# Kernel optimization log

Hardware: AMD Instinct MI355X
Metric: run time of the kernel (lower is better)

## Reference

```python
import jax, jax.numpy as jnp
import numpy as np
from jax import lax

SEQ, B, NF, NC, D, NO, L = 2036, 32, 64, 100, 512, 4, 2048
EPS = 1e-5


def leaky(x):
    return jnp.where(x > 0, x, 0.2 * x)


def conv1d(x, w, b):
    # x: [B, Cin, L], w: [Cout, Cin, K] -> [B, Cout, L-K+1] (VALID)
    y = lax.conv_general_dilated(x, w, (1,), 'VALID',
                                 dimension_numbers=('NCH', 'OIH', 'NCH'))
    return y + b[None, :, None]


def maxpool3(x):
    # kernel 3, stride 1, VALID, over last dim
    return lax.reduce_window(x, -jnp.inf, lax.max, (1, 1, 3), (1, 1, 1), 'VALID')


def layernorm(x, g, b):
    m = jnp.mean(x, -1, keepdims=True)
    v = jnp.mean(jnp.square(x - m), -1, keepdims=True)
    return (x - m) * lax.rsqrt(v + EPS) * g + b


def setup_inputs() -> dict:
    key = jax.random.key(0)
    ks = jax.random.split(key, 16)
    s = 0.02
    return {
        'input': jax.random.normal(ks[0], (SEQ, B, NF), jnp.float32),
        'history': jax.random.normal(ks[1], (B, NO, L), jnp.float32),
        'static': jax.random.normal(ks[2], (B, NC), jnp.float32),
        'W_feat': jax.random.normal(ks[3], (D, NF), jnp.float32) * s,
        'b_feat': jnp.zeros((D,), jnp.float32),
        'w1': jax.random.normal(ks[4], (D // 4, NO, 3), jnp.float32) * s,
        'b1': jnp.zeros((D // 4,), jnp.float32),
        'w2': jax.random.normal(ks[5], (D // 2, D // 4, 3), jnp.float32) * s,
        'b2': jnp.zeros((D // 2,), jnp.float32),
        'w3': jax.random.normal(ks[6], (D, D // 2, 3), jnp.float32) * s,
        'b3': jnp.zeros((D,), jnp.float32),
        'g1': jnp.ones((D,), jnp.float32),
        'beta1': jnp.zeros((D,), jnp.float32),
        'W_city': jax.random.normal(ks[7], (D, NC), jnp.float32) * s,
        'b_city': jnp.zeros((D,), jnp.float32),
        'g2': jnp.ones((D,), jnp.float32),
        'beta2': jnp.zeros((D,), jnp.float32),
    }


def reference(input, history, static, W_feat, b_feat, w1, b1, w2, b2, w3, b3,
              g1, beta1, W_city, b_city, g2, beta2):
    # feat embed: [S, B, NF] @ [NF, D]
    x = leaky(jnp.einsum('sbf,df->sbd', input, W_feat) + b_feat)
    # conv/pool stack on history [B, NO, L]
    h = maxpool3(leaky(conv1d(history, w1, b1)))
    h = maxpool3(leaky(conv1d(h, w2, b2)))
    h = maxpool3(leaky(conv1d(h, w3, b3)))            # [B, D, S]
    x = x + jnp.transpose(h, (2, 0, 1))               # [S, B, D]
    x = layernorm(x, g1, beta1)
    # diag_embed(city_embed(static)) matmul == broadcasted elementwise scale
    c = static @ W_city.T + b_city                    # [B, D]
    x = x * c[None, :, :]
    x = layernorm(x, g2, beta2)
    return x
```

## Files before the change

kernel.cpp:

```cpp
#include <hip/hip_runtime.h>
#include <hip/hip_bf16.h>

#define SEQ 2036
#define BB 32
#define DDIM 512

typedef __attribute__((ext_vector_type(4))) float f32x4;
typedef __attribute__((ext_vector_type(8))) short bf16x8v;
typedef __attribute__((ext_vector_type(8))) unsigned short u16x8;
typedef __attribute__((ext_vector_type(4))) unsigned short u16x4;

__device__ __forceinline__ float leaky_f(float x) { return x > 0.f ? x : 0.2f * x; }
__device__ __forceinline__ unsigned short f2bf(float x) {
    unsigned u = __float_as_uint(x);
    return (unsigned short)((u + 0x7fffu + ((u >> 16) & 1u)) >> 16);
}
__device__ __forceinline__ float bf2f(unsigned short h) { return __uint_as_float(((unsigned)h) << 16); }

#define GLOAD_LDS16(g, l)                                                                  \
    __builtin_amdgcn_global_load_lds((__attribute__((address_space(1))) const unsigned int*)(g), \
                                     (__attribute__((address_space(3))) unsigned int*)(l), 16, 0, 0)

__global__ void transpose_w_kernel(const float* __restrict__ w, float* __restrict__ wT,
                                   int Dout, int K3) {
    int i = blockIdx.x * blockDim.x + threadIdx.x;
    if (i < Dout * K3) {
        int d = i / K3, k = i - d * K3;
        wT[k * Dout + d] = w[i];
    }
}

__global__ void prep_w_kernel(const float* __restrict__ w, __hip_bfloat16* __restrict__ wp,
                              int CIN, int NB) {
    int idx = blockIdx.x * 256 + threadIdx.x;
    int NQ = CIN >> 5;
    int total = 3 * NQ * NB * 4096;
    if (idx >= total) return;
    int o = idx & 4095, tile = idx >> 12;
    int nb = tile % NB;
    int tmp = tile / NB;
    int q = tmp % NQ, k = tmp / NQ;
    int n = o >> 5, low = o & 31;
    int cs = low >> 3, j = low & 7;
    int c = cs ^ ((n >> 1) & 3);
    int kk = (c << 3) | j;
    float v = w[((size_t)(nb * 128 + n)) * CIN * 3 + (q * 32 + kk) * 3 + k];
    ((unsigned short*)wp)[idx] = f2bf(v);
}

__global__ void prep_wf_kernel(const float* __restrict__ Wf, __hip_bfloat16* __restrict__ wfP) {
    int idx = blockIdx.x * 256 + threadIdx.x;
    int e = idx & 7;
    int l = (idx >> 3) & 63;
    int frag = idx >> 9;
    int q = frag >> 5, j = frag & 31;
    int n = l & 15, g = l >> 4;
    ((unsigned short*)wfP)[idx] = f2bf(Wf[(j * 16 + n) * 64 + q * 32 + g * 8 + e]);
}

__global__ void city_kernel(const float* __restrict__ st, const float* __restrict__ Wc,
                            const float* __restrict__ bc, float* __restrict__ c) {
    int b = blockIdx.x, d = threadIdx.x;
    const float* sb = st + b * 100;
    float acc = bc[d];
#pragma unroll 4
    for (int f = 0; f < 100; ++f) acc = fmaf(sb[f], Wc[d * 100 + f], acc);
    c[b * DDIM + d] = acc;
}

__global__ __launch_bounds__(128) void conv1_kernel(const float* __restrict__ in,
                                                    const float* __restrict__ wT,
                                                    const float* __restrict__ bias,
                                                    __hip_bfloat16* __restrict__ out) {
    const int b = blockIdx.y, s0 = blockIdx.x * 32, d = threadIdx.x;
    __shared__ float tile[4][36];
    const float* inb = in + (size_t)b * 4 * 2048;
    for (int i = threadIdx.x; i < 4 * 36; i += 128) {
        int cin = i / 36, p = i - cin * 36;
        int s = s0 + p;
        tile[cin][p] = (s < 2048) ? inb[cin * 2048 + s] : 0.f;
    }
    __syncthreads();
    float acc[34];
#pragma unroll
    for (int i = 0; i < 34; ++i) acc[i] = 0.f;
#pragma unroll
    for (int cin = 0; cin < 4; ++cin) {
        float w0 = wT[(cin * 3 + 0) * 128 + d];
        float w1 = wT[(cin * 3 + 1) * 128 + d];
        float w2 = wT[(cin * 3 + 2) * 128 + d];
        float r0 = tile[cin][0], r1 = tile[cin][1];
#pragma unroll
        for (int p = 0; p < 34; ++p) {
            float r2 = tile[cin][p + 2];
            acc[p] = fmaf(r0, w0, fmaf(r1, w1, fmaf(r2, w2, acc[p])));
            r0 = r1; r1 = r2;
        }
    }
    float bvv = bias[d];
    unsigned short* o16 = (unsigned short*)out;
#pragma unroll
    for (int i = 0; i < 32; ++i) {
        int sp = s0 + i;
        if (sp < 2044) {
            float v = leaky_f(fmaxf(fmaxf(acc[i], acc[i + 1]), acc[i + 2]) + bvv);
            o16[((size_t)b * 2044 + sp) * 128 + d] = f2bf(v);
        }
    }
}

template <int CIN, int DOUT>
__global__ __launch_bounds__(256, 3) void conv_mfma_kernel(
    const __hip_bfloat16* __restrict__ hin,
    const __hip_bfloat16* __restrict__ wprep,
    const float* __restrict__ bias,
    __hip_bfloat16* __restrict__ hout,
    int Lin, int Lpool, long bstride, long sstride)
{
    constexpr int NQ = CIN / 32;
    constexpr int HALVES = (CIN + 127) / 128;
    constexpr int NSTEP = 3 * NQ;
    constexpr int SPH = NSTEP / HALVES;
    constexpr int NBL = DOUT / 128;

    __shared__ __attribute__((aligned(16))) unsigned char smem[34816 + 16384];
    unsigned char* panel = smem;
    unsigned char* cstage = smem;
    unsigned char* bls = smem + 34816;

    const int t = threadIdx.x;
    const int lane = t & 63, w = t >> 6;
    const int wr = w >> 1, wn = w & 1;
    const int l15 = lane & 15, lg = lane >> 4;

    const int nwg = gridDim.x;
    const int lw = (blockIdx.x & 7) * (nwg >> 3) + (blockIdx.x >> 3);
    const int nb = lw % NBL;
    const int tmp = lw / NBL;
    const int st = tmp % 17;
    const int b = tmp / 17;
    const int s0 = st * 126;

    auto stage_panel = [&](int half) {
        const char* srcb = (const char*)hin + (((size_t)b * Lin) * CIN + half * 128) * 2;
#pragma unroll
        for (int iter = 0; iter < 8; ++iter) {
            int chunk = iter * 256 + t;
            int r = chunk >> 4, cd = chunk & 15;
            int c = (cd & 8) | ((cd ^ r) & 7);
            int row = s0 + r; if (row > Lin - 1) row = Lin - 1;
            const char* src = srcb + ((size_t)row * CIN + c * 8) * 2;
            GLOAD_LDS16(src, panel + (iter * 256 + w * 64) * 16);
        }
        if (t < 32) {
            int chunk = 2048 + t;
            int r = chunk >> 4, cd = chunk & 15;
            int c = (cd & 8) | ((cd ^ r) & 7);
            int row = s0 + r; if (row > Lin - 1) row = Lin - 1;
            const char* src = srcb + ((size_t)row * CIN + c * 8) * 2;
            GLOAD_LDS16(src, panel + 2048 * 16);
        }
    };
    auto stage_b = [&](int ss, int bi) {
        int k = (ss % SPH) >> 2;
        int qg = (ss / SPH) * 4 + (ss & 3);
        int tile = (k * NQ + qg) * NBL + nb;
        const char* src = (const char*)wprep + (size_t)tile * 8192;
        char* dst = (char*)bls + bi * 8192;
        GLOAD_LDS16(src + t * 16, dst + (w << 10));
        GLOAD_LDS16(src + 4096 + t * 16, dst + 4096 + (w << 10));
    };

    f32x4 acc[4][4];
#pragma unroll
    for (int i = 0; i < 4; ++i)
#pragma unroll
        for (int j = 0; j < 4; ++j) acc[i][j] = (f32x4){0.f, 0.f, 0.f, 0.f};

    stage_panel(0);
    stage_b(0, 0);
    __syncthreads();

    int boff[4];
#pragma unroll
    for (int nf = 0; nf < 4; ++nf) {
        int n = wn * 64 + nf * 16 + l15;
        boff[nf] = n * 64 + ((lg ^ ((n >> 1) & 3)) << 4);
    }
    const int rbse = wr * 64 + l15;

    for (int ss = 0; ss < NSTEP; ++ss) {
        const int bi = ss & 1;
        if (ss + 1 < NSTEP) stage_b(ss + 1, bi ^ 1);
        const int k = (ss % SPH) >> 2;
        const int cc = (ss & 3) * 4 + lg;
        bf16x8v a[4], bfr[4];
#pragma unroll
        for (int mf = 0; mf < 4; ++mf) {
            int r = rbse + mf * 16 + k;
            int csw = (cc & 8) | ((cc ^ r) & 7);
            a[mf] = *(const bf16x8v*)(panel + r * 256 + (csw << 4));
        }
#pragma unroll
        for (int nf = 0; nf < 4; ++nf)
            bfr[nf] = *(const bf16x8v*)(bls + bi * 8192 + boff[nf]);
#pragma unroll
        for (int mf = 0; mf < 4; ++mf)
#pragma unroll
            for (int nf = 0; nf < 4; ++nf)
                acc[mf][nf] = __builtin_amdgcn_mfma_f32_16x16x32_bf16(a[mf], bfr[nf], acc[mf][nf], 0, 0, 0);
        __syncthreads();
        if (HALVES == 2 && ss == SPH - 1) {
            stage_panel(1);
            __syncthreads();
        }
    }

#pragma unroll
    for (int mf = 0; mf < 4; ++mf) {
        int srow = wr * 64 + mf * 16 + (lg << 2);
#pragma unroll
        for (int nf = 0; nf < 4; ++nf) {
            int n = wn * 64 + nf * 16 + l15;
            f32x4 v = acc[mf][nf];
            unsigned lo = (unsigned)f2bf(v.x) | ((unsigned)f2bf(v.y) << 16);
            unsigned hi = (unsigned)f2bf(v.z) | ((unsigned)f2bf(v.w) << 16);
            *(uint2*)(cstage + (size_t)n * 272 + srow * 2) = make_uint2(lo, hi);
        }
    }
    __syncthreads();

    const int n = t & 127, h = t >> 7;
    const float bv = bias[nb * 128 + n];
    const int SP = (Lpool - s0 < 126) ? (Lpool - s0) : 126;
    const int splo = h ? 63 : 0;
    const int sphim = h ? 126 : 63;
    const int sphi = (SP < sphim) ? SP : sphim;
    const int cbg = h ? 7 : 0, ceg = h ? 16 : 9;
    unsigned short* outp = (unsigned short*)hout;
    const size_t obase = (size_t)b * bstride + (size_t)s0 * sstride + nb * 128 + n;
    float p2 = 0.f, p1 = 0.f;
    for (int j = cbg; j < ceg; ++j) {
        u16x8 ch = *(const u16x8*)(cstage + (size_t)n * 272 + (j << 4));
#pragma unroll
        for (int i = 0; i < 8; ++i) {
            float cur = bf2f(ch[i]);
            int sp = j * 8 + i - 2;
            if (sp >= splo && sp < sphi) {
                float v = fmaxf(fmaxf(p2, p1), cur) + bv;
                outp[obase + (size_t)sp * sstride] = f2bf(leaky_f(v));
            }
            p2 = p1; p1 = cur;
        }
    }
}

#define XSTR 514
__global__ __launch_bounds__(256, 4) void epi_mfma3_kernel(
    const float* __restrict__ input,
    const __hip_bfloat16* __restrict__ wfP,
    const float* __restrict__ bfeat,
    const __hip_bfloat16* __restrict__ h3,
    const float* __restrict__ cvec,
    const float* __restrict__ g1, const float* __restrict__ be1,
    const float* __restrict__ g2, const float* __restrict__ be2,
    float* __restrict__ outp)
{
    __shared__ float x_lds[16 * XSTR];
    const int t = threadIdx.x;
    const int lane = t & 63, w = t >> 6;
    const int l15 = lane & 15, lg = lane >> 4;
    const long r0 = (long)blockIdx.x * 16;

    f32x4 acc[8];
#pragma unroll
    for (int jl = 0; jl < 8; ++jl) acc[jl] = (f32x4){0.f, 0.f, 0.f, 0.f};

    const unsigned short* wp = (const unsigned short*)wfP;
#pragma unroll
    for (int q = 0; q < 2; ++q) {
        const f32x4* ap = (const f32x4*)(input + (r0 + l15) * 64 + q * 32 + lg * 8);
        f32x4 a0 = ap[0];
        f32x4 a1 = ap[1];
        bf16x8v af;
        af[0] = (short)f2bf(a0.x); af[1] = (short)f2bf(a0.y);
        af[2] = (short)f2bf(a0.z); af[3] = (short)f2bf(a0.w);
        af[4] = (short)f2bf(a1.x); af[5] = (short)f2bf(a1.y);
        af[6] = (short)f2bf(a1.z); af[7] = (short)f2bf(a1.w);
#pragma unroll
        for (int jl = 0; jl < 8; ++jl) {
            int frag = q * 32 + w * 8 + jl;
            bf16x8v bfr = *(const bf16x8v*)(wp + ((size_t)frag * 64 + lane) * 8);
            acc[jl] = __builtin_amdgcn_mfma_f32_16x16x32_bf16(af, bfr, acc[jl], 0, 0, 0);
        }
    }

#pragma unroll
    for (int jl = 0; jl < 8; ++jl) {
        int d = (w * 8 + jl) * 16 + l15;
        float bfv = bfeat[d];
#pragma unroll
        for (int i = 0; i < 4; ++i) {
            int row = lg * 4 + i;
            x_lds[row * XSTR + d] = leaky_f(acc[jl][i] + bfv);
        }
    }
    __syncthreads();

    const unsigned short* h3u = (const unsigned short*)h3;
    const int l4 = lane * 4;
    f32x4 g1a = *(const f32x4*)(g1 + l4);
    f32x4 g1b = *(const f32x4*)(g1 + 256 + l4);
    f32x4 b1a = *(const f32x4*)(be1 + l4);
    f32x4 b1b = *(const f32x4*)(be1 + 256 + l4);
    f32x4 g2a = *(const f32x4*)(g2 + l4);
    f32x4 g2b = *(const f32x4*)(g2 + 256 + l4);
    f32x4 b2a = *(const f32x4*)(be2 + l4);
    f32x4 b2b = *(const f32x4*)(be2 + 256 + l4);

    for (int rr = 0; rr < 4; ++rr) {
        int row = w * 4 + rr;
        long r = r0 + row;
        int b = (int)(r & 31);
        f32x4 xa = *(const f32x4*)(x_lds + row * XSTR + l4);
        f32x4 xb = *(const f32x4*)(x_lds + row * XSTR + 256 + l4);
        u16x4 ha = *(const u16x4*)(h3u + r * 512 + l4);
        u16x4 hb = *(const u16x4*)(h3u + r * 512 + 256 + l4);
        float v[8];
        float s = 0.f;
#pragma unroll
        for (int e = 0; e < 4; ++e) {
            v[e] = xa[e] + bf2f(ha[e]);
            v[4 + e] = xb[e] + bf2f(hb[e]);
            s += v[e] + v[4 + e];
        }
#pragma unroll
        for (int off = 32; off; off >>= 1) s += __shfl_xor(s, off);
        float m = s * (1.f / 512.f);
        float vs = 0.f;
#pragma unroll
        for (int j = 0; j < 8; ++j) { float dd = v[j] - m; vs += dd * dd; }
#pragma unroll
        for (int off = 32; off; off >>= 1) vs += __shfl_xor(vs, off);
        float rstd = rsqrtf(vs * (1.f / 512.f) + 1e-5f);

        f32x4 ca = *(const f32x4*)(cvec + b * 512 + l4);
        f32x4 cb = *(const f32x4*)(cvec + b * 512 + 256 + l4);
        float z[8]; float s2 = 0.f;
#pragma unroll
        for (int e = 0; e < 4; ++e) {
            z[e] = ((v[e] - m) * rstd * g1a[e] + b1a[e]) * ca[e];
            z[4 + e] = ((v[4 + e] - m) * rstd * g1b[e] + b1b[e]) * cb[e];
            s2 += z[e] + z[4 + e];
        }
#pragma unroll
        for (int off = 32; off; off >>= 1) s2 += __shfl_xor(s2, off);
        float m2 = s2 * (1.f / 512.f);
        float vs2 = 0.f;
#pragma unroll
        for (int j = 0; j < 8; ++j) { float dd = z[j] - m2; vs2 += dd * dd; }
#pragma unroll
        for (int off = 32; off; off >>= 1) vs2 += __shfl_xor(vs2, off);
        float rstd2 = rsqrtf(vs2 * (1.f / 512.f) + 1e-5f);

        f32x4 oa, ob;
#pragma unroll
        for (int e = 0; e < 4; ++e) {
            oa[e] = (z[e] - m2) * rstd2 * g2a[e] + b2a[e];
            ob[e] = (z[4 + e] - m2) * rstd2 * g2b[e] + b2b[e];
        }
        __builtin_nontemporal_store(oa, (f32x4*)(outp + r * 512 + l4));
        __builtin_nontemporal_store(ob, (f32x4*)(outp + r * 512 + 256 + l4));
    }
}

extern "C" void kernel_launch(void* const* d_in, const int* in_sizes, int n_in,
                              void* d_out, int out_size, void* d_ws, size_t ws_size,
                              hipStream_t stream) {
    const float* input   = (const float*)d_in[0];
    const float* history = (const float*)d_in[1];
    const float* stat    = (const float*)d_in[2];
    const float* W_feat  = (const float*)d_in[3];
    const float* b_feat  = (const float*)d_in[4];
    const float* w1      = (const float*)d_in[5];
    const float* b1      = (const float*)d_in[6];
    const float* w2      = (const float*)d_in[7];
    const float* b2      = (const float*)d_in[8];
    const float* w3      = (const float*)d_in[9];
    const float* b3      = (const float*)d_in[10];
    const float* g1      = (const float*)d_in[11];
    const float* beta1   = (const float*)d_in[12];
    const float* W_city  = (const float*)d_in[13];
    const float* b_city  = (const float*)d_in[14];
    const float* g2      = (const float*)d_in[15];
    const float* beta2   = (const float*)d_in[16];
    float* out = (float*)d_out;

    char* wsb = (char*)d_ws;
    size_t off = 0;
    auto alloc = [&](size_t bytes) {
        void* p = wsb + off;
        off = (off + bytes + 255) & ~(size_t)255;
        return p;
    };
    __hip_bfloat16* h1  = (__hip_bfloat16*)alloc((size_t)BB * 2044 * 128 * 2);
    __hip_bfloat16* h2  = (__hip_bfloat16*)alloc((size_t)BB * 2040 * 256 * 2);
    __hip_bfloat16* h3  = (__hip_bfloat16*)alloc((size_t)SEQ * BB * 512 * 2);
    float*          cv  = (float*)alloc((size_t)BB * DDIM * 4);
    float*          w1T = (float*)alloc(12 * 128 * 4);
    __hip_bfloat16* w2P = (__hip_bfloat16*)alloc((size_t)3 * 4 * 2 * 4096 * 2);
    __hip_bfloat16* w3P = (__hip_bfloat16*)alloc((size_t)3 * 8 * 4 * 4096 * 2);
    __hip_bfloat16* wfP = (__hip_bfloat16*)alloc((size_t)64 * 512 * 2);

    transpose_w_kernel<<<(12 * 128 + 255) / 256, 256, 0, stream>>>(w1, w1T, 128, 12);
    prep_w_kernel<<<(3 * 4 * 2 * 4096) / 256, 256, 0, stream>>>(w2, w2P, 128, 2);
    prep_w_kernel<<<(3 * 8 * 4 * 4096) / 256, 256, 0, stream>>>(w3, w3P, 256, 4);
    prep_wf_kernel<<<(64 * 512) / 256, 256, 0, stream>>>(W_feat, wfP);
    city_kernel<<<BB, DDIM, 0, stream>>>(stat, W_city, b_city, cv);

    conv1_kernel<<<dim3(64, BB), 128, 0, stream>>>(history, w1T, b1, h1);
    conv_mfma_kernel<128, 256><<<17 * 2 * BB, 256, 0, stream>>>(
        h1, w2P, b2, h2, 2044, 2040, 2040L * 256, 256);
    conv_mfma_kernel<256, 512><<<17 * 4 * BB, 256, 0, stream>>>(
        h2, w3P, b3, h3, 2040, 2036, 512, 32L * 512);

    epi_mfma3_kernel<<<(SEQ * BB) / 16, 256, 0, stream>>>(
        input, wfP, b_feat, h3, cv, g1, beta1, g2, beta2, out);
}
```

Measured before the change: 179.6 us.

## Load conv weight fragments directly from global in MFMA fragment order

Pre-packs the conv2/conv3 weights into per-lane MFMA B-fragment order so each wave reads its B operands with coalesced 16-byte global loads. This removes the double-buffered LDS staging of weights and the per-k-step __syncthreads. The LDS footprint drops to the activation panel, and launch bounds rise to 4 blocks per SM for higher occupancy. The cost is that weight loads are no longer prefetched a step ahead, so each MFMA step waits on global or L2 latency, and every wave reloads its fragments through cache.

```diff
diff --git a/kernel.cpp b/kernel.cpp
--- a/kernel.cpp
+++ b/kernel.cpp
@@ -30,22 +30,25 @@
     }
 }
 
-__global__ void prep_w_kernel(const float* __restrict__ w, __hip_bfloat16* __restrict__ wp,
-                              int CIN, int NB) {
+__global__ void prep_wb_kernel(const float* __restrict__ w, __hip_bfloat16* __restrict__ wb,
+                               int CIN, int NBL, int total) {
     int idx = blockIdx.x * 256 + threadIdx.x;
+    if (idx >= total) return;
     int NQ = CIN >> 5;
-    int total = 3 * NQ * NB * 4096;
-    if (idx >= total) return;
-    int o = idx & 4095, tile = idx >> 12;
-    int nb = tile % NB;
-    int tmp = tile / NB;
-    int q = tmp % NQ, k = tmp / NQ;
-    int n = o >> 5, low = o & 31;
-    int cs = low >> 3, j = low & 7;
-    int c = cs ^ ((n >> 1) & 3);
-    int kk = (c << 3) | j;
-    float v = w[((size_t)(nb * 128 + n)) * CIN * 3 + (q * 32 + kk) * 3 + k];
-    ((unsigned short*)wp)[idx] = f2bf(v);
+    int NSTEP = 3 * NQ;
+    int HALVES = (CIN + 127) / 128;
+    int SPH = NSTEP / HALVES;
+    int e = idx & 7;
+    int l = (idx >> 3) & 63;
+    int nf = (idx >> 9) & 3;
+    int wn = (idx >> 11) & 1;
+    int rest = idx >> 12;
+    int nb = rest % NBL, ss = rest / NBL;
+    int k = (ss % SPH) >> 2;
+    int qg = (ss / SPH) * 4 + (ss & 3);
+    int n = nb * 128 + wn * 64 + nf * 16 + (l & 15);
+    int cin = qg * 32 + (l >> 4) * 8 + e;
+    ((unsigned short*)wb)[idx] = f2bf(w[(size_t)n * CIN * 3 + cin * 3 + k]);
 }
 
 __global__ void prep_wf_kernel(const float* __restrict__ Wf, __hip_bfloat16* __restrict__ wfP) {
@@ -110,9 +113,9 @@
 }
 
 template <int CIN, int DOUT>
-__global__ __launch_bounds__(256, 3) void conv_mfma_kernel(
+__global__ __launch_bounds__(256, 4) void conv_mfma_kernel(
     const __hip_bfloat16* __restrict__ hin,
-    const __hip_bfloat16* __restrict__ wprep,
+    const __hip_bfloat16* __restrict__ wb,
     const float* __restrict__ bias,
     __hip_bfloat16* __restrict__ hout,
     int Lin, int Lpool, long bstride, long sstride)
@@ -123,10 +126,9 @@
     constexpr int SPH = NSTEP / HALVES;
     constexpr int NBL = DOUT / 128;
 
-    __shared__ __attribute__((aligned(16))) unsigned char smem[34816 + 16384];
+    __shared__ __attribute__((aligned(16))) unsigned char smem[34816];
     unsigned char* panel = smem;
     unsigned char* cstage = smem;
-    unsigned char* bls = smem + 34816;
 
     const int t = threadIdx.x;
     const int lane = t & 63, w = t >> 6;
@@ -161,15 +163,6 @@
             GLOAD_LDS16(src, panel + 2048 * 16);
         }
     };
-    auto stage_b = [&](int ss, int bi) {
-        int k = (ss % SPH) >> 2;
-        int qg = (ss / SPH) * 4 + (ss & 3);
-        int tile = (k * NQ + qg) * NBL + nb;
-        const char* src = (const char*)wprep + (size_t)tile * 8192;
-        char* dst = (char*)bls + bi * 8192;
-        GLOAD_LDS16(src + t * 16, dst + (w << 10));
-        GLOAD_LDS16(src + 4096 + t * 16, dst + 4096 + (w << 10));
-    };
 
     f32x4 acc[4][4];
 #pragma unroll
@@ -177,24 +170,18 @@
 #pragma unroll
         for (int j = 0; j < 4; ++j) acc[i][j] = (f32x4){0.f, 0.f, 0.f, 0.f};
 
-    stage_panel(0);
-    stage_b(0, 0);
-    __syncthreads();
-
-    int boff[4];
-#pragma unroll
-    for (int nf = 0; nf < 4; ++nf) {
-        int n = wn * 64 + nf * 16 + l15;
-        boff[nf] = n * 64 + ((lg ^ ((n >> 1) & 3)) << 4);
-    }
     const int rbse = wr * 64 + l15;
-
-    for (int ss = 0; ss < NSTEP; ++ss) {
-        const int bi = ss & 1;
-        if (ss + 1 < NSTEP) stage_b(ss + 1, bi ^ 1);
+    const unsigned short* wbp = (const unsigned short*)wb;
+
+    auto kstep = [&](int ss) {
         const int k = (ss % SPH) >> 2;
         const int cc = (ss & 3) * 4 + lg;
+        const unsigned short* wq =
+            wbp + (((size_t)ss * NBL + nb) * 2 + wn) * 2048 + (size_t)lane * 8;
         bf16x8v a[4], bfr[4];
+#pragma unroll
+        for (int nf = 0; nf < 4; ++nf)
+            bfr[nf] = *(const bf16x8v*)(wq + nf * 512);
 #pragma unroll
         for (int mf = 0; mf < 4; ++mf) {
             int r = rbse + mf * 16 + k;
@@ -202,19 +189,22 @@
             a[mf] = *(const bf16x8v*)(panel + r * 256 + (csw << 4));
         }
 #pragma unroll
-        for (int nf = 0; nf < 4; ++nf)
-            bfr[nf] = *(const bf16x8v*)(bls + bi * 8192 + boff[nf]);
-#pragma unroll
         for (int mf = 0; mf < 4; ++mf)
 #pragma unroll
             for (int nf = 0; nf < 4; ++nf)
                 acc[mf][nf] = __builtin_amdgcn_mfma_f32_16x16x32_bf16(a[mf], bfr[nf], acc[mf][nf], 0, 0, 0);
+    };
+
+    stage_panel(0);
+    __syncthreads();
+    for (int ss = 0; ss < SPH; ++ss) kstep(ss);
+    if (HALVES == 2) {
         __syncthreads();
-        if (HALVES == 2 && ss == SPH - 1) {
-            stage_panel(1);
-            __syncthreads();
-        }
-    }
+        stage_panel(1);
+        __syncthreads();
+        for (int ss = SPH; ss < NSTEP; ++ss) kstep(ss);
+    }
+    __syncthreads();
 
 #pragma unroll
     for (int mf = 0; mf < 4; ++mf) {
@@ -408,21 +398,21 @@
     __hip_bfloat16* h3  = (__hip_bfloat16*)alloc((size_t)SEQ * BB * 512 * 2);
     float*          cv  = (float*)alloc((size_t)BB * DDIM * 4);
     float*          w1T = (float*)alloc(12 * 128 * 4);
-    __hip_bfloat16* w2P = (__hip_bfloat16*)alloc((size_t)3 * 4 * 2 * 4096 * 2);
-    __hip_bfloat16* w3P = (__hip_bfloat16*)alloc((size_t)3 * 8 * 4 * 4096 * 2);
+    __hip_bfloat16* wb2 = (__hip_bfloat16*)alloc((size_t)12 * 2 * 8 * 512 * 2);
+    __hip_bfloat16* wb3 = (__hip_bfloat16*)alloc((size_t)24 * 4 * 8 * 512 * 2);
     __hip_bfloat16* wfP = (__hip_bfloat16*)alloc((size_t)64 * 512 * 2);
 
     transpose_w_kernel<<<(12 * 128 + 255) / 256, 256, 0, stream>>>(w1, w1T, 128, 12);
-    prep_w_kernel<<<(3 * 4 * 2 * 4096) / 256, 256, 0, stream>>>(w2, w2P, 128, 2);
-    prep_w_kernel<<<(3 * 8 * 4 * 4096) / 256, 256, 0, stream>>>(w3, w3P, 256, 4);
+    prep_wb_kernel<<<(12 * 2 * 8 * 512) / 256, 256, 0, stream>>>(w2, wb2, 128, 2, 12 * 2 * 8 * 512);
+    prep_wb_kernel<<<(24 * 4 * 8 * 512) / 256, 256, 0, stream>>>(w3, wb3, 256, 4, 24 * 4 * 8 * 512);
     prep_wf_kernel<<<(64 * 512) / 256, 256, 0, stream>>>(W_feat, wfP);
     city_kernel<<<BB, DDIM, 0, stream>>>(stat, W_city, b_city, cv);
 
     conv1_kernel<<<dim3(64, BB), 128, 0, stream>>>(history, w1T, b1, h1);
     conv_mfma_kernel<128, 256><<<17 * 2 * BB, 256, 0, stream>>>(
-        h1, w2P, b2, h2, 2044, 2040, 2040L * 256, 256);
+        h1, wb2, b2, h2, 2044, 2040, 2040L * 256, 256);
     conv_mfma_kernel<256, 512><<<17 * 4 * BB, 256, 0, stream>>>(
-        h2, w3P, b3, h3, 2040, 2036, 512, 32L * 512);
+        h2, wb3, b3, h3, 2040, 2036, 512, 32L * 512);
 
     epi_mfma3_kernel<<<(SEQ * BB) / 16, 256, 0, stream>>>(
         input, wfP, b_feat, h3, cv, g1, beta1, g2, beta2, out);
```

Measured after the change: 191.6 us. 1.07x slower.

## Load conv3 weight fragments directly from global and fuse prep kernels

Applied to the files above, without the earlier changes.

Merges the five small weight-prep and city-embedding kernels into one launch, which removes launch overhead. For the conv3 layer, weights are pre-packed into per-lane MFMA fragment order and read straight from global/L2 into registers, so there is no LDS double-buffering and no per-step barrier. This frees 16 KB of LDS and raises the occupancy target to 4 blocks. The cost is that global-load latency now sits directly in front of each MFMA step, and weight reads are no longer shared through LDS across the workgroup.

```diff
diff --git a/kernel.cpp b/kernel.cpp
--- a/kernel.cpp
+++ b/kernel.cpp
@@ -21,51 +21,68 @@
     __builtin_amdgcn_global_load_lds((__attribute__((address_space(1))) const unsigned int*)(g), \
                                      (__attribute__((address_space(3))) unsigned int*)(l), 16, 0, 0)
 
-__global__ void transpose_w_kernel(const float* __restrict__ w, float* __restrict__ wT,
-                                   int Dout, int K3) {
-    int i = blockIdx.x * blockDim.x + threadIdx.x;
-    if (i < Dout * K3) {
-        int d = i / K3, k = i - d * K3;
-        wT[k * Dout + d] = w[i];
-    }
-}
-
-__global__ void prep_w_kernel(const float* __restrict__ w, __hip_bfloat16* __restrict__ wp,
-                              int CIN, int NB) {
+__global__ __launch_bounds__(256) void prep_all_kernel(
+    const float* __restrict__ w1, float* __restrict__ w1T,
+    const float* __restrict__ w2, __hip_bfloat16* __restrict__ w2P,
+    const float* __restrict__ w3, __hip_bfloat16* __restrict__ wb3,
+    const float* __restrict__ Wf, __hip_bfloat16* __restrict__ wfP,
+    const float* __restrict__ st, const float* __restrict__ Wc,
+    const float* __restrict__ bc, float* __restrict__ cv)
+{
     int idx = blockIdx.x * 256 + threadIdx.x;
-    int NQ = CIN >> 5;
-    int total = 3 * NQ * NB * 4096;
-    if (idx >= total) return;
-    int o = idx & 4095, tile = idx >> 12;
-    int nb = tile % NB;
-    int tmp = tile / NB;
-    int q = tmp % NQ, k = tmp / NQ;
-    int n = o >> 5, low = o & 31;
-    int cs = low >> 3, j = low & 7;
-    int c = cs ^ ((n >> 1) & 3);
-    int kk = (c << 3) | j;
-    float v = w[((size_t)(nb * 128 + n)) * CIN * 3 + (q * 32 + kk) * 3 + k];
-    ((unsigned short*)wp)[idx] = f2bf(v);
-}
-
-__global__ void prep_wf_kernel(const float* __restrict__ Wf, __hip_bfloat16* __restrict__ wfP) {
-    int idx = blockIdx.x * 256 + threadIdx.x;
-    int e = idx & 7;
-    int l = (idx >> 3) & 63;
-    int frag = idx >> 9;
-    int q = frag >> 5, j = frag & 31;
-    int n = l & 15, g = l >> 4;
-    ((unsigned short*)wfP)[idx] = f2bf(Wf[(j * 16 + n) * 64 + q * 32 + g * 8 + e]);
-}
-
-__global__ void city_kernel(const float* __restrict__ st, const float* __restrict__ Wc,
-                            const float* __restrict__ bc, float* __restrict__ c) {
-    int b = blockIdx.x, d = threadIdx.x;
-    const float* sb = st + b * 100;
-    float acc = bc[d];
+    if (idx < 1536) {
+        int d = idx / 12, k = idx - d * 12;
+        w1T[k * 128 + d] = w1[idx];
+        return;
+    }
+    idx -= 1536;
+    if (idx < 98304) {
+        int o = idx & 4095, tile = idx >> 12;
+        int nb = tile % 2;
+        int tmp = tile / 2;
+        int q = tmp % 4, k = tmp / 4;
+        int n = o >> 5, low = o & 31;
+        int cs = low >> 3, j = low & 7;
+        int c = cs ^ ((n >> 1) & 3);
+        int kk = (c << 3) | j;
+        float v = w2[((size_t)(nb * 128 + n)) * 128 * 3 + (q * 32 + kk) * 3 + k];
+        ((unsigned short*)w2P)[idx] = f2bf(v);
+        return;
+    }
+    idx -= 98304;
+    if (idx < 393216) {
+        int e = idx & 7;
+        int l = (idx >> 3) & 63;
+        int nf = (idx >> 9) & 3;
+        int wn = (idx >> 11) & 1;
+        int rest = idx >> 12;
+        int nb = rest % 4, ss = rest / 4;
+        int k = (ss % 12) >> 2;
+        int qg = (ss / 12) * 4 + (ss & 3);
+        int n = nb * 128 + wn * 64 + nf * 16 + (l & 15);
+        int cin = qg * 32 + (l >> 4) * 8 + e;
+        ((unsigned short*)wb3)[idx] = f2bf(w3[(size_t)n * 256 * 3 + cin * 3 + k]);
+        return;
+    }
+    idx -= 393216;
+    if (idx < 32768) {
+        int e = idx & 7;
+        int l = (idx >> 3) & 63;
+        int frag = idx >> 9;
+        int q = frag >> 5, j = frag & 31;
+        int n = l & 15, g = l >> 4;
+        ((unsigned short*)wfP)[idx] = f2bf(Wf[(j * 16 + n) * 64 + q * 32 + g * 8 + e]);
+        return;
+    }
+    idx -= 32768;
+    if (idx < 16384) {
+        int b = idx >> 9, d = idx & 511;
+        const float* sb = st + b * 100;
+        float acc = bc[d];
 #pragma unroll 4
-    for (int f = 0; f < 100; ++f) acc = fmaf(sb[f], Wc[d * 100 + f], acc);
-    c[b * DDIM + d] = acc;
+        for (int f = 0; f < 100; ++f) acc = fmaf(sb[f], Wc[d * 100 + f], acc);
+        cv[b * 512 + d] = acc;
+    }
 }
 
 __global__ __launch_bounds__(128) void conv1_kernel(const float* __restrict__ in,
@@ -109,8 +126,8 @@
     }
 }
 
-template <int CIN, int DOUT>
-__global__ __launch_bounds__(256, 3) void conv_mfma_kernel(
+template <int CIN, int DOUT, bool LDSB>
+__global__ __launch_bounds__(256, LDSB ? 3 : 4) void conv_mfma_kernel(
     const __hip_bfloat16* __restrict__ hin,
     const __hip_bfloat16* __restrict__ wprep,
     const float* __restrict__ bias,
@@ -122,8 +139,9 @@
     constexpr int NSTEP = 3 * NQ;
     constexpr int SPH = NSTEP / HALVES;
     constexpr int NBL = DOUT / 128;
-
-    __shared__ __attribute__((aligned(16))) unsigned char smem[34816 + 16384];
+    constexpr int SMEM = LDSB ? (34816 + 16384) : 34816;
+
+    __shared__ __attribute__((aligned(16))) unsigned char smem[SMEM];
     unsigned char* panel = smem;
     unsigned char* cstage = smem;
     unsigned char* bls = smem + 34816;
@@ -161,15 +179,6 @@
             GLOAD_LDS16(src, panel + 2048 * 16);
         }
     };
-    auto stage_b = [&](int ss, int bi) {
-        int k = (ss % SPH) >> 2;
-        int qg = (ss / SPH) * 4 + (ss & 3);
-        int tile = (k * NQ + qg) * NBL + nb;
-        const char* src = (const char*)wprep + (size_t)tile * 8192;
-        char* dst = (char*)bls + bi * 8192;
-        GLOAD_LDS16(src + t * 16, dst + (w << 10));
-        GLOAD_LDS16(src + 4096 + t * 16, dst + 4096 + (w << 10));
-    };
 
     f32x4 acc[4][4];
 #pragma unroll
@@ -177,43 +186,87 @@
 #pragma unroll
         for (int j = 0; j < 4; ++j) acc[i][j] = (f32x4){0.f, 0.f, 0.f, 0.f};
 
-    stage_panel(0);
-    stage_b(0, 0);
-    __syncthreads();
-
-    int boff[4];
-#pragma unroll
-    for (int nf = 0; nf < 4; ++nf) {
-        int n = wn * 64 + nf * 16 + l15;
-        boff[nf] = n * 64 + ((lg ^ ((n >> 1) & 3)) << 4);
-    }
     const int rbse = wr * 64 + l15;
 
-    for (int ss = 0; ss < NSTEP; ++ss) {
-        const int bi = ss & 1;
-        if (ss + 1 < NSTEP) stage_b(ss + 1, bi ^ 1);
-        const int k = (ss % SPH) >> 2;
-        const int cc = (ss & 3) * 4 + lg;
-        bf16x8v a[4], bfr[4];
-#pragma unroll
-        for (int mf = 0; mf < 4; ++mf) {
-            int r = rbse + mf * 16 + k;
-            int csw = (cc & 8) | ((cc ^ r) & 7);
-            a[mf] = *(const bf16x8v*)(panel + r * 256 + (csw << 4));
-        }
-#pragma unroll
-        for (int nf = 0; nf < 4; ++nf)
-            bfr[nf] = *(const bf16x8v*)(bls + bi * 8192 + boff[nf]);
-#pragma unroll
-        for (int mf = 0; mf < 4; ++mf)
+    if (LDSB) {
+        auto stage_b = [&](int ss, int bi) {
+            int k = (ss % SPH) >> 2;
+            int qg = (ss / SPH) * 4 + (ss & 3);
+            int tile = (k * NQ + qg) * NBL + nb;
+            const char* src = (const char*)wprep + (size_t)tile * 8192;
+            char* dst = (char*)bls + bi * 8192;
+            GLOAD_LDS16(src + t * 16, dst + (w << 10));
+            GLOAD_LDS16(src + 4096 + t * 16, dst + 4096 + (w << 10));
+        };
+        stage_panel(0);
+        stage_b(0, 0);
+        __syncthreads();
+        int boff[4];
+#pragma unroll
+        for (int nf = 0; nf < 4; ++nf) {
+            int n = wn * 64 + nf * 16 + l15;
+            boff[nf] = n * 64 + ((lg ^ ((n >> 1) & 3)) << 4);
+        }
+        for (int ss = 0; ss < NSTEP; ++ss) {
+            const int bi = ss & 1;
+            if (ss + 1 < NSTEP) stage_b(ss + 1, bi ^ 1);
+            const int k = (ss % SPH) >> 2;
+            const int cc = (ss & 3) * 4 + lg;
+            bf16x8v a[4], bfr[4];
+#pragma unroll
+            for (int mf = 0; mf < 4; ++mf) {
+                int r = rbse + mf * 16 + k;
+                int csw = (cc & 8) | ((cc ^ r) & 7);
+                a[mf] = *(const bf16x8v*)(panel + r * 256 + (csw << 4));
+            }
 #pragma unroll
             for (int nf = 0; nf < 4; ++nf)
-                acc[mf][nf] = __builtin_amdgcn_mfma_f32_16x16x32_bf16(a[mf], bfr[nf], acc[mf][nf], 0, 0, 0);
+                bfr[nf] = *(const bf16x8v*)(bls + bi * 8192 + boff[nf]);
+#pragma unroll
+            for (int mf = 0; mf < 4; ++mf)
+#pragma unroll
+                for (int nf = 0; nf < 4; ++nf)
+                    acc[mf][nf] = __builtin_amdgcn_mfma_f32_16x16x32_bf16(a[mf], bfr[nf], acc[mf][nf], 0, 0, 0);
+            __syncthreads();
+            if (HALVES == 2 && ss == SPH - 1) {
+                stage_panel(1);
+                __syncthreads();
+            }
+        }
         __syncthreads();
-        if (HALVES == 2 && ss == SPH - 1) {
+    } else {
+        const unsigned short* wbp = (const unsigned short*)wprep;
+        auto kstep = [&](int ss) {
+            const int k = (ss % SPH) >> 2;
+            const int cc = (ss & 3) * 4 + lg;
+            const unsigned short* wq =
+                wbp + (((size_t)ss * NBL + nb) * 2 + wn) * 2048 + (size_t)lane * 8;
+            bf16x8v a[4], bfr[4];
+#pragma unroll
+            for (int nf = 0; nf < 4; ++nf)
+                bfr[nf] = *(const bf16x8v*)(wq + nf * 512);
+#pragma unroll
+            for (int mf = 0; mf < 4; ++mf) {
+                int r = rbse + mf * 16 + k;
+                int csw = (cc & 8) | ((cc ^ r) & 7);
+                a[mf] = *(const bf16x8v*)(panel + r * 256 + (csw << 4));
+            }
+#pragma unroll
+            for (int mf = 0; mf < 4; ++mf)
+#pragma unroll
+                for (int nf = 0; nf < 4; ++nf)
+                    acc[mf][nf] = __builtin_amdgcn_mfma_f32_16x16x32_bf16(a[mf], bfr[nf], acc[mf][nf], 0, 0, 0);
+        };
+        stage_panel(0);
+        __syncthreads();
+        for (int ss = 0; ss < SPH; ++ss) kstep(ss);
+        if (HALVES == 2) {
+            __syncthreads();
             stage_panel(1);
             __syncthreads();
-        }
+            for (int ss = SPH; ss < NSTEP; ++ss) kstep(ss);
+        }
+        __syncthreads();
     }
 
 #pragma unroll
@@ -408,21 +461,18 @@
     __hip_bfloat16* h3  = (__hip_bfloat16*)alloc((size_t)SEQ * BB * 512 * 2);
     float*          cv  = (float*)alloc((size_t)BB * DDIM * 4);
     float*          w1T = (float*)alloc(12 * 128 * 4);
-    __hip_bfloat16* w2P = (__hip_bfloat16*)alloc((size_t)3 * 4 * 2 * 4096 * 2);
-    __hip_bfloat16* w3P = (__hip_bfloat16*)alloc((size_t)3 * 8 * 4 * 4096 * 2);
-    __hip_bfloat16* wfP = (__hip_bfloat16*)alloc((size_t)64 * 512 * 2);
-
-    transpose_w_kernel<<<(12 * 128 + 255) / 256, 256, 0, stream>>>(w1, w1T, 128, 12);
-    prep_w_kernel<<<(3 * 4 * 2 * 4096) / 256, 256, 0, stream>>>(w2, w2P, 128, 2);
-    prep_w_kernel<<<(3 * 8 * 4 * 4096) / 256, 256, 0, stream>>>(w3, w3P, 256, 4);
-    prep_wf_kernel<<<(64 * 512) / 256, 256, 0, stream>>>(W_feat, wfP);
-    city_kernel<<<BB, DDIM, 0, stream>>>(stat, W_city, b_city, cv);
+    __hip_bfloat16* w2P = (__hip_bfloat16*)alloc((size_t)98304 * 2);
+    __hip_bfloat16* wb3 = (__hip_bfloat16*)alloc((size_t)393216 * 2);
+    __hip_bfloat16* wfP = (__hip_bfloat16*)alloc((size_t)32768 * 2);
+
+    prep_all_kernel<<<(542208 + 255) / 256, 256, 0, stream>>>(
+        w1, w1T, w2, w2P, w3, wb3, W_feat, wfP, stat, W_city, b_city, cv);
 
     conv1_kernel<<<dim3(64, BB), 128, 0, stream>>>(history, w1T, b1, h1);
-    conv_mfma_kernel<128, 256><<<17 * 2 * BB, 256, 0, stream>>>(
+    conv_mfma_kernel<128, 256, true><<<17 * 2 * BB, 256, 0, stream>>>(
         h1, w2P, b2, h2, 2044, 2040, 2040L * 256, 256);
-    conv_mfma_kernel<256, 512><<<17 * 4 * BB, 256, 0, stream>>>(
-        h2, w3P, b3, h3, 2040, 2036, 512, 32L * 512);
+    conv_mfma_kernel<256, 512, false><<<17 * 4 * BB, 256, 0, stream>>>(
+        h2, wb3, b3, h3, 2040, 2036, 512, 32L * 512);
 
     epi_mfma3_kernel<<<(SEQ * BB) / 16, 256, 0, stream>>>(
         input, wfP, b_feat, h3, cv, g1, beta1, g2, beta2, out);
```

Result: no change. 177.2 us (-1.3%).
